# Kernel tuning notes

Hardware: AMD Instinct MI355X
Metric: run time of the kernel (lower is better)

Reference implementation:

```python
import jax, jax.numpy as jnp
import numpy as np


def _dF(field, c):
    """Central differences of component c of field [B,X,Y,Z,C] -> [B,X-2,Y-2,Z-2,3]."""
    f = field[..., c]
    dx = (f[:, 2:, 1:-1, 1:-1] - f[:, :-2, 1:-1, 1:-1]) * 0.5
    dy = (f[:, 1:-1, 2:, 1:-1] - f[:, 1:-1, :-2, 1:-1]) * 0.5
    dz = (f[:, 1:-1, 1:-1, 2:] - f[:, 1:-1, 1:-1, :-2]) * 0.5
    return jnp.stack((dx, dy, dz), axis=4)


def setup_inputs() -> dict:
    key = jax.random.key(0)
    grid = jax.random.normal(key, (2, 160, 160, 160, 3), dtype=jnp.float32)
    return {"grid": grid}


def reference(grid):
    # First derivatives of each displacement component: [B,X-2,Y-2,Z-2,3]
    dx = _dF(grid, 0)
    dy = _dF(grid, 1)
    dz = _dF(grid, 2)
    # Second derivatives: [B,X-4,Y-4,Z-4,3]
    dxx = _dF(dx, 0)
    dyy = _dF(dy, 1)
    dzz = _dF(dz, 2)
    dxy = _dF(dx, 1)
    dyz = _dF(dy, 2)
    dxz = _dF(dx, 2)
    penalty = jnp.sum(dxx ** 2 + dyy ** 2 + dzz ** 2
                      + 2.0 * (dxy ** 2 + dyz ** 2 + dxz ** 2))
    return penalty / dxx.size
```

## Files before the change

### kernel.cpp

```cpp
#include <hip/hip_runtime.h>

#define OY 480
#define OX 76800
#define SB 12288000
#define JT 12
#define KT 39
#define IT 39
#define NBLK 416
#define ROWF 129
#define RW 132
#define NROW 16
#define SLICE (NROW*RW)
#define NBUF 6
#define SLICE_FLOATS (NROW*ROWF)
#define PTS (JT*KT)
#define INV_SIZE (1.0f/22778496.0f)

__global__ __launch_bounds__(512)
void be_partials(const float* __restrict__ g, float* __restrict__ partial) {
    __shared__ float lds[NBUF * SLICE];
    __shared__ float wsum[8];

    const int tid = threadIdx.x;
    const int bid = blockIdx.x;
    const int kt  = bid & 3;
    const int is  = (bid >> 2) & 3;
    const int r   = bid >> 4;
    const int jt  = r % 13;
    const int bb  = r / 13;

    const int j0  = jt * JT;
    const int k0z = kt * KT;
    const int ib  = is * IT;

    const float* __restrict__ G = g + (size_t)bb * SB;

    int gd0, gd1, gd2, gd3, gd4 = 0, ld0, ld1, ld2, ld3, ld4 = 0;
    {
        int f, row, pos;
        f = tid;        row = f / ROWF; pos = f - row * ROWF;
        gd0 = (j0 + row) * OY + k0z * 3 + pos;  ld0 = row * RW + pos;
        f = tid + 512;  row = f / ROWF; pos = f - row * ROWF;
        gd1 = (j0 + row) * OY + k0z * 3 + pos;  ld1 = row * RW + pos;
        f = tid + 1024; row = f / ROWF; pos = f - row * ROWF;
        gd2 = (j0 + row) * OY + k0z * 3 + pos;  ld2 = row * RW + pos;
        f = tid + 1536; row = f / ROWF; pos = f - row * ROWF;
        gd3 = (j0 + row) * OY + k0z * 3 + pos;  ld3 = row * RW + pos;
    }
    const bool tail = (tid < SLICE_FLOATS - 2048);
    if (tail) {
        int f = tid + 2048; int row = f / ROWF; int pos = f - row * ROWF;
        gd4 = (j0 + row) * OY + k0z * 3 + pos;  ld4 = row * RW + pos;
    }

    const bool act = tid < PTS;
    int jj = tid / KT;
    int kk = tid - jj * KT;
    if (!act) { jj = 0; kk = 0; }
    const int cbase = (jj + 2) * RW + (kk + 2) * 3;

    #pragma unroll
    for (int w = 0; w < 5; ++w) {
        const int x = ib + w;
        const float* base = G + (size_t)x * OX;
        float a0 = base[gd0], a1 = base[gd1], a2 = base[gd2], a3 = base[gd3];
        float a4 = tail ? base[gd4] : 0.0f;
        float* L = lds + (x % NBUF) * SLICE;
        L[ld0] = a0; L[ld1] = a1; L[ld2] = a2; L[ld3] = a3;
        if (tail) L[ld4] = a4;
    }
    __syncthreads();

    float s = 0.0f;
    for (int i0 = ib; i0 < ib + IT; ++i0) {
        const int xn = i0 + 5;
        const bool doLoad = (xn <= ib + 42);
        float a0 = 0.f, a1 = 0.f, a2 = 0.f, a3 = 0.f, a4 = 0.f;
        if (doLoad) {
            const float* base = G + (size_t)xn * OX;
            a0 = base[gd0]; a1 = base[gd1]; a2 = base[gd2]; a3 = base[gd3];
            if (tail) a4 = base[gd4];
        }

        if (act) {
            int s0 = i0 % NBUF;
            int s1 = s0 + 1; if (s1 >= NBUF) s1 -= NBUF;
            int s2 = s1 + 1; if (s2 >= NBUF) s2 -= NBUF;
            int s3 = s2 + 1; if (s3 >= NBUF) s3 -= NBUF;
            int s4 = s3 + 1; if (s4 >= NBUF) s4 -= NBUF;
            const float* Sm2 = lds + s0 * SLICE + cbase;
            const float* Sm1 = lds + s1 * SLICE + cbase;
            const float* Sc  = lds + s2 * SLICE + cbase;
            const float* Sp1 = lds + s3 * SLICE + cbase;
            const float* Sp2 = lds + s4 * SLICE + cbase;

            const float c0 = Sc[0], c1 = Sc[1], c2 = Sc[2];
            float hzz0 = Sc[6] - 2.0f*c0 + Sc[-6];
            float hzz1 = Sc[7] - 2.0f*c1 + Sc[-5];
            float hzz2 = Sc[8] - 2.0f*c2 + Sc[-4];
            float hyy0 = Sc[ 2*RW]     - 2.0f*c0 + Sc[-2*RW];
            float hyy1 = Sc[ 2*RW + 1] - 2.0f*c1 + Sc[-2*RW + 1];
            float hxx0 = Sp2[0] - 2.0f*c0 + Sm2[0];
            float hyz0 = (Sc[RW+3] - Sc[RW-3]) - (Sc[-RW+3] - Sc[-RW-3]);
            float hyz1 = (Sc[RW+4] - Sc[RW-2]) - (Sc[-RW+4] - Sc[-RW-2]);
            float hyz2 = (Sc[RW+5] - Sc[RW-1]) - (Sc[-RW+5] - Sc[-RW-1]);
            float hxy0 = (Sp1[ RW]   - Sp1[-RW])   - (Sm1[ RW]   - Sm1[-RW]);
            float hxy1 = (Sp1[ RW+1] - Sp1[-RW+1]) - (Sm1[ RW+1] - Sm1[-RW+1]);
            float hxz0 = (Sp1[3] - Sp1[-3]) - (Sm1[3] - Sm1[-3]);
            float hxz1 = (Sp1[4] - Sp1[-2]) - (Sm1[4] - Sm1[-2]);
            float hxz2 = (Sp1[5] - Sp1[-1]) - (Sm1[5] - Sm1[-1]);

            float w1 = hxx0*hxx0;
            w1 = fmaf(hyy1, hyy1, w1); w1 = fmaf(hzz2, hzz2, w1);
            w1 = fmaf(hxy1, hxy1, w1); w1 = fmaf(hxz2, hxz2, w1);
            w1 = fmaf(hyz2, hyz2, w1);
            float w2 = hyy0*hyy0;
            w2 = fmaf(hzz0, hzz0, w2); w2 = fmaf(hzz1, hzz1, w2);
            w2 = fmaf(hxz1, hxz1, w2);
            float w3 = hxy0*hxy0;
            w3 = fmaf(hxz0, hxz0, w3); w3 = fmaf(hyz1, hyz1, w3);
            float w4 = hyz0*hyz0;

            float t = fmaf(2.0f, w2, w1);
            t = fmaf(3.0f, w3, t);
            t = fmaf(4.0f, w4, t);
            s = fmaf(0.0625f, t, s);
        }

        if (doLoad) {
            float* L = lds + (xn % NBUF) * SLICE;
            L[ld0] = a0; L[ld1] = a1; L[ld2] = a2; L[ld3] = a3;
            if (tail) L[ld4] = a4;
        }
        __syncthreads();
    }

    #pragma unroll
    for (int off = 32; off > 0; off >>= 1) s += __shfl_down(s, off, 64);
    if ((tid & 63) == 0) wsum[tid >> 6] = s;
    __syncthreads();
    if (tid == 0) {
        float tot = 0.0f;
        #pragma unroll
        for (int w = 0; w < 8; ++w) tot += wsum[w];
        partial[bid] = tot;
    }
}

__global__ __launch_bounds__(256)
void be_final(const float* __restrict__ partial, float* __restrict__ out) {
    float s = 0.0f;
    for (int i = threadIdx.x; i < NBLK; i += 256) s += partial[i];
    #pragma unroll
    for (int off = 32; off > 0; off >>= 1) s += __shfl_down(s, off, 64);
    __shared__ float ws[4];
    if ((threadIdx.x & 63) == 0) ws[threadIdx.x >> 6] = s;
    __syncthreads();
    if (threadIdx.x == 0)
        out[0] = ((ws[0] + ws[1]) + (ws[2] + ws[3])) * INV_SIZE;
}

extern "C" void kernel_launch(void* const* d_in, const int* in_sizes, int n_in,
                              void* d_out, int out_size, void* d_ws, size_t ws_size,
                              hipStream_t stream) {
    const float* grid = (const float*)d_in[0];
    float* out = (float*)d_out;
    float* partials = (float*)d_ws;

    be_partials<<<dim3(NBLK), dim3(512), 0, stream>>>(grid, partials);
    be_final<<<1, 256, 0, stream>>>(partials, out);
}
```

Measured before the change: 171.3 us.

## Restructure stencil with SoA LDS layout, double buffering, and x-derivative register reuse

Rewrites the partial kernel so global rows are loaded as float4 and transposed into a component-major (SoA) shared layout. The kernel now keeps only two slices in LDS and carries x-direction first differences and previous centre values in registers across steps instead of reading five slices. Each thread handles four z points with vectorised LDS reads, and the grid changes to 1014 blocks of 256 threads with shorter x-slabs. This is meant to cut LDS traffic and footprint and raise occupancy, at the cost of more halo reloading from shorter x-tiles and heavier register use.

```diff
diff --git a/kernel.cpp b/kernel.cpp
--- a/kernel.cpp
+++ b/kernel.cpp
@@ -4,147 +4,179 @@
 #define OX 76800
 #define SB 12288000
 #define JT 12
-#define KT 39
-#define IT 39
-#define NBLK 416
-#define ROWF 129
-#define RW 132
+#define KQ 13
+#define IT 12
 #define NROW 16
-#define SLICE (NROW*RW)
-#define NBUF 6
-#define SLICE_FLOATS (NROW*ROWF)
-#define PTS (JT*KT)
+#define ZST 60
+#define RST 180
+#define SLICE (NROW*RST)
+#define CTHR (JT*KQ)
+#define NGRP (NROW*14)
+#define NBLK 1014
 #define INV_SIZE (1.0f/22778496.0f)
 
-__global__ __launch_bounds__(512)
+__device__ __forceinline__ float4 ld4p(const float* p){ return *reinterpret_cast<const float4*>(p); }
+__device__ __forceinline__ float2 ld2p(const float* p){ return *reinterpret_cast<const float2*>(p); }
+__device__ __forceinline__ void st4p(float* p, float4 v){ *reinterpret_cast<float4*>(p) = v; }
+
+#define STEP(P, V0a, V0b, DP) { \
+    const int s = 2*d + (P); \
+    const bool doLoad = stg && (s <= 14); \
+    float4 A4, B4, C4; \
+    if (doLoad) { \
+        const float* gp = G + (size_t)(i0 - 1 + s)*OX + gbase; \
+        A4 = ld4p(gp); B4 = ld4p(gp+4); C4 = ld4p(gp+8); \
+    } \
+    if (act) { \
+        const bool doWS = (s >= 2) && (s <= 13); \
+        const bool doXY = (s >= 3) && (s <= 14); \
+        const bool doXX = (s >= 4); \
+        const float* L = lds + (P)*SLICE; \
+        float v0c[4], dz0[4], dz1[4], dz2[4], dyc0[4], dyc1[4]; \
+        {  \
+          float4 lo = ld4p(L+oj), hi = ld4p(L+oj+4); \
+          float f[8] = {lo.x,lo.y,lo.z,lo.w,hi.x,hi.y,hi.z,hi.w}; \
+          _Pragma("unroll") for (int v=0;v<4;++v){ v0c[v]=f[v+2]; dz0[v]=f[v+3]-f[v+1]; } \
+          if (doWS) { \
+            _Pragma("unroll") for (int v=0;v<4;++v){ float h=f[v+4]-2.f*f[v+2]+f[v]; cls2=fmaf(h,h,cls2); } \
+            float2 pa=ld2p(L+oj+2*RST+2), pb=ld2p(L+oj+2*RST+4); \
+            float2 ma=ld2p(L+oj-2*RST+2), mb=ld2p(L+oj-2*RST+4); \
+            float hp[4]={pa.x,pa.y,pb.x,pb.y}, hm[4]={ma.x,ma.y,mb.x,mb.y}; \
+            _Pragma("unroll") for (int v=0;v<4;++v){ float h=hp[v]-2.f*f[v+2]+hm[v]; cls2=fmaf(h,h,cls2); } \
+          } \
+        } \
+        {  \
+          float4 lo = ld4p(L+oj+ZST), hi = ld4p(L+oj+ZST+4); \
+          float f[8] = {lo.x,lo.y,lo.z,lo.w,hi.x,hi.y,hi.z,hi.w}; \
+          _Pragma("unroll") for (int v=0;v<4;++v){ dz1[v]=f[v+3]-f[v+1]; } \
+          if (doWS) { \
+            _Pragma("unroll") for (int v=0;v<4;++v){ float h=f[v+4]-2.f*f[v+2]+f[v]; cls2=fmaf(h,h,cls2); } \
+            float2 pa=ld2p(L+oj+2*RST+ZST+2), pb=ld2p(L+oj+2*RST+ZST+4); \
+            float2 ma=ld2p(L+oj-2*RST+ZST+2), mb=ld2p(L+oj-2*RST+ZST+4); \
+            float hp[4]={pa.x,pa.y,pb.x,pb.y}, hm[4]={ma.x,ma.y,mb.x,mb.y}; \
+            _Pragma("unroll") for (int v=0;v<4;++v){ float h=hp[v]-2.f*f[v+2]+hm[v]; cls1=fmaf(h,h,cls1); } \
+          } \
+        } \
+        {  \
+          float4 lo = ld4p(L+oj+2*ZST), hi = ld4p(L+oj+2*ZST+4); \
+          float f[8] = {lo.x,lo.y,lo.z,lo.w,hi.x,hi.y,hi.z,hi.w}; \
+          _Pragma("unroll") for (int v=0;v<4;++v){ dz2[v]=f[v+3]-f[v+1]; } \
+          if (doWS) { \
+            _Pragma("unroll") for (int v=0;v<4;++v){ float h=f[v+4]-2.f*f[v+2]+f[v]; cls1=fmaf(h,h,cls1); } \
+          } \
+        } \
+        {  \
+          float4 plo=ld4p(L+oj+RST), phi=ld4p(L+oj+RST+4); \
+          float4 mlo=ld4p(L+oj-RST), mhi=ld4p(L+oj-RST+4); \
+          float dyw[6]={plo.y-mlo.y, plo.z-mlo.z, plo.w-mlo.w, phi.x-mhi.x, phi.y-mhi.y, phi.z-mhi.z}; \
+          _Pragma("unroll") for (int v=0;v<4;++v) dyc0[v]=dyw[v+1]; \
+          if (doWS) { _Pragma("unroll") for (int v=0;v<4;++v){ float h=dyw[v+2]-dyw[v]; cls4=fmaf(h,h,cls4); } } \
+        } \
+        {  \
+          float4 plo=ld4p(L+oj+RST+ZST), phi=ld4p(L+oj+RST+ZST+4); \
+          float4 mlo=ld4p(L+oj-RST+ZST), mhi=ld4p(L+oj-RST+ZST+4); \
+          float dyw[6]={plo.y-mlo.y, plo.z-mlo.z, plo.w-mlo.w, phi.x-mhi.x, phi.y-mhi.y, phi.z-mhi.z}; \
+          _Pragma("unroll") for (int v=0;v<4;++v) dyc1[v]=dyw[v+1]; \
+          if (doWS) { _Pragma("unroll") for (int v=0;v<4;++v){ float h=dyw[v+2]-dyw[v]; cls3=fmaf(h,h,cls3); } } \
+        } \
+        if (doWS) {  \
+          float4 plo=ld4p(L+oj+RST+2*ZST), phi=ld4p(L+oj+RST+2*ZST+4); \
+          float4 mlo=ld4p(L+oj-RST+2*ZST), mhi=ld4p(L+oj-RST+2*ZST+4); \
+          float dyw[6]={plo.y-mlo.y, plo.z-mlo.z, plo.w-mlo.w, phi.x-mhi.x, phi.y-mhi.y, phi.z-mhi.z}; \
+          _Pragma("unroll") for (int v=0;v<4;++v){ float h=dyw[v+2]-dyw[v]; cls1=fmaf(h,h,cls1); } \
+        } \
+        _Pragma("unroll") for (int v=0;v<4;++v) { \
+          float o0=DP[0][v], o1=DP[1][v], o2=DP[2][v], o3=DP[3][v], o4=DP[4][v]; \
+          if (doXY) { float h; \
+            h=dyc0[v]-o0; cls3=fmaf(h,h,cls3); \
+            h=dyc1[v]-o1; cls1=fmaf(h,h,cls1); \
+            h=dz0[v]-o2;  cls3=fmaf(h,h,cls3); \
+            h=dz1[v]-o3;  cls2=fmaf(h,h,cls2); \
+            h=dz2[v]-o4;  cls1=fmaf(h,h,cls1); \
+          } \
+          DP[0][v]=dyc0[v]; DP[1][v]=dyc1[v]; DP[2][v]=dz0[v]; DP[3][v]=dz1[v]; DP[4][v]=dz2[v]; \
+          float w2v=V0a[v], w4v=V0b[v]; \
+          if (doXX) { float h=v0c[v]-2.f*w2v+w4v; cls1=fmaf(h,h,cls1); } \
+          V0b[v]=w2v; V0a[v]=v0c[v]; \
+        } \
+    } \
+    if (doLoad) { \
+        float* Lw = lds + ((P)^1)*SLICE + lbase; \
+        st4p(Lw,       make_float4(A4.x,A4.w,B4.z,C4.y)); \
+        st4p(Lw+ZST,   make_float4(A4.y,B4.x,B4.w,C4.z)); \
+        st4p(Lw+2*ZST, make_float4(A4.z,B4.y,C4.x,C4.w)); \
+    } \
+    __syncthreads(); \
+}
+
+__global__ __launch_bounds__(256)
 void be_partials(const float* __restrict__ g, float* __restrict__ partial) {
-    __shared__ float lds[NBUF * SLICE];
-    __shared__ float wsum[8];
+    __shared__ float lds[2*SLICE];
+    __shared__ float wsum[4];
 
     const int tid = threadIdx.x;
     const int bid = blockIdx.x;
-    const int kt  = bid & 3;
-    const int is  = (bid >> 2) & 3;
-    const int r   = bid >> 4;
-    const int jt  = r % 13;
-    const int bb  = r / 13;
-
-    const int j0  = jt * JT;
-    const int k0z = kt * KT;
-    const int ib  = is * IT;
-
-    const float* __restrict__ G = g + (size_t)bb * SB;
-
-    int gd0, gd1, gd2, gd3, gd4 = 0, ld0, ld1, ld2, ld3, ld4 = 0;
-    {
-        int f, row, pos;
-        f = tid;        row = f / ROWF; pos = f - row * ROWF;
-        gd0 = (j0 + row) * OY + k0z * 3 + pos;  ld0 = row * RW + pos;
-        f = tid + 512;  row = f / ROWF; pos = f - row * ROWF;
-        gd1 = (j0 + row) * OY + k0z * 3 + pos;  ld1 = row * RW + pos;
-        f = tid + 1024; row = f / ROWF; pos = f - row * ROWF;
-        gd2 = (j0 + row) * OY + k0z * 3 + pos;  ld2 = row * RW + pos;
-        f = tid + 1536; row = f / ROWF; pos = f - row * ROWF;
-        gd3 = (j0 + row) * OY + k0z * 3 + pos;  ld3 = row * RW + pos;
-    }
-    const bool tail = (tid < SLICE_FLOATS - 2048);
-    if (tail) {
-        int f = tid + 2048; int row = f / ROWF; int pos = f - row * ROWF;
-        gd4 = (j0 + row) * OY + k0z * 3 + pos;  ld4 = row * RW + pos;
-    }
-
-    const bool act = tid < PTS;
-    int jj = tid / KT;
-    int kk = tid - jj * KT;
-    if (!act) { jj = 0; kk = 0; }
-    const int cbase = (jj + 2) * RW + (kk + 2) * 3;
-
+    const int is = bid % 13;
+    int r1 = bid / 13;
+    const int kt = r1 % 3; r1 /= 3;
+    const int jt = r1 % 13;
+    const int bb = r1 / 13;
+
+    const int j0  = 2 + jt*JT;
+    const int zlo = 52*kt;
+    const int i0  = 2 + is*IT;
+    const float* __restrict__ G = g + (size_t)bb*SB;
+
+    const bool stg = tid < NGRP;
+    int gbase = 0, lbase = 0;
+    if (stg) {
+        int rr = tid/14, zq = tid - (tid/14)*14;
+        gbase = (j0-2+rr)*OY + (zlo+4*zq)*3;
+        lbase = rr*RST + 4*zq;
+    }
+
+    const bool act = tid < CTHR;
+    int cj = tid/KQ, cq = tid - (tid/KQ)*KQ;
+    if (!act) { cj = 0; cq = 0; }
+    const int oj = (cj+2)*RST + 4*cq;
+
+    float v0A0[4], v0A1[4], v0B0[4], v0B1[4];
+    float dpA[5][4], dpB[5][4];
     #pragma unroll
-    for (int w = 0; w < 5; ++w) {
-        const int x = ib + w;
-        const float* base = G + (size_t)x * OX;
-        float a0 = base[gd0], a1 = base[gd1], a2 = base[gd2], a3 = base[gd3];
-        float a4 = tail ? base[gd4] : 0.0f;
-        float* L = lds + (x % NBUF) * SLICE;
-        L[ld0] = a0; L[ld1] = a1; L[ld2] = a2; L[ld3] = a3;
-        if (tail) L[ld4] = a4;
+    for (int v=0;v<4;++v){
+        v0A0[v]=v0A1[v]=v0B0[v]=v0B1[v]=0.f;
+        #pragma unroll
+        for (int q=0;q<5;++q){ dpA[q][v]=0.f; dpB[q][v]=0.f; }
+    }
+    float cls1=0.f, cls2=0.f, cls3=0.f, cls4=0.f;
+
+    if (stg) {
+        const float* gp = G + (size_t)(i0-2)*OX + gbase;
+        float4 A4 = ld4p(gp), B4 = ld4p(gp+4), C4 = ld4p(gp+8);
+        float* Lw = lds + lbase;
+        st4p(Lw,       make_float4(A4.x,A4.w,B4.z,C4.y));
+        st4p(Lw+ZST,   make_float4(A4.y,B4.x,B4.w,C4.z));
+        st4p(Lw+2*ZST, make_float4(A4.z,B4.y,C4.x,C4.w));
     }
     __syncthreads();
 
-    float s = 0.0f;
-    for (int i0 = ib; i0 < ib + IT; ++i0) {
-        const int xn = i0 + 5;
-        const bool doLoad = (xn <= ib + 42);
-        float a0 = 0.f, a1 = 0.f, a2 = 0.f, a3 = 0.f, a4 = 0.f;
-        if (doLoad) {
-            const float* base = G + (size_t)xn * OX;
-            a0 = base[gd0]; a1 = base[gd1]; a2 = base[gd2]; a3 = base[gd3];
-            if (tail) a4 = base[gd4];
-        }
-
-        if (act) {
-            int s0 = i0 % NBUF;
-            int s1 = s0 + 1; if (s1 >= NBUF) s1 -= NBUF;
-            int s2 = s1 + 1; if (s2 >= NBUF) s2 -= NBUF;
-            int s3 = s2 + 1; if (s3 >= NBUF) s3 -= NBUF;
-            int s4 = s3 + 1; if (s4 >= NBUF) s4 -= NBUF;
-            const float* Sm2 = lds + s0 * SLICE + cbase;
-            const float* Sm1 = lds + s1 * SLICE + cbase;
-            const float* Sc  = lds + s2 * SLICE + cbase;
-            const float* Sp1 = lds + s3 * SLICE + cbase;
-            const float* Sp2 = lds + s4 * SLICE + cbase;
-
-            const float c0 = Sc[0], c1 = Sc[1], c2 = Sc[2];
-            float hzz0 = Sc[6] - 2.0f*c0 + Sc[-6];
-            float hzz1 = Sc[7] - 2.0f*c1 + Sc[-5];
-            float hzz2 = Sc[8] - 2.0f*c2 + Sc[-4];
-            float hyy0 = Sc[ 2*RW]     - 2.0f*c0 + Sc[-2*RW];
-            float hyy1 = Sc[ 2*RW + 1] - 2.0f*c1 + Sc[-2*RW + 1];
-            float hxx0 = Sp2[0] - 2.0f*c0 + Sm2[0];
-            float hyz0 = (Sc[RW+3] - Sc[RW-3]) - (Sc[-RW+3] - Sc[-RW-3]);
-            float hyz1 = (Sc[RW+4] - Sc[RW-2]) - (Sc[-RW+4] - Sc[-RW-2]);
-            float hyz2 = (Sc[RW+5] - Sc[RW-1]) - (Sc[-RW+5] - Sc[-RW-1]);
-            float hxy0 = (Sp1[ RW]   - Sp1[-RW])   - (Sm1[ RW]   - Sm1[-RW]);
-            float hxy1 = (Sp1[ RW+1] - Sp1[-RW+1]) - (Sm1[ RW+1] - Sm1[-RW+1]);
-            float hxz0 = (Sp1[3] - Sp1[-3]) - (Sm1[3] - Sm1[-3]);
-            float hxz1 = (Sp1[4] - Sp1[-2]) - (Sm1[4] - Sm1[-2]);
-            float hxz2 = (Sp1[5] - Sp1[-1]) - (Sm1[5] - Sm1[-1]);
-
-            float w1 = hxx0*hxx0;
-            w1 = fmaf(hyy1, hyy1, w1); w1 = fmaf(hzz2, hzz2, w1);
-            w1 = fmaf(hxy1, hxy1, w1); w1 = fmaf(hxz2, hxz2, w1);
-            w1 = fmaf(hyz2, hyz2, w1);
-            float w2 = hyy0*hyy0;
-            w2 = fmaf(hzz0, hzz0, w2); w2 = fmaf(hzz1, hzz1, w2);
-            w2 = fmaf(hxz1, hxz1, w2);
-            float w3 = hxy0*hxy0;
-            w3 = fmaf(hxz0, hxz0, w3); w3 = fmaf(hyz1, hyz1, w3);
-            float w4 = hyz0*hyz0;
-
-            float t = fmaf(2.0f, w2, w1);
-            t = fmaf(3.0f, w3, t);
-            t = fmaf(4.0f, w4, t);
-            s = fmaf(0.0625f, t, s);
-        }
-
-        if (doLoad) {
-            float* L = lds + (xn % NBUF) * SLICE;
-            L[ld0] = a0; L[ld1] = a1; L[ld2] = a2; L[ld3] = a3;
-            if (tail) L[ld4] = a4;
-        }
-        __syncthreads();
-    }
+    #pragma unroll 1
+    for (int d = 0; d < 8; ++d) {
+        STEP(0, v0A0, v0A1, dpA)
+        STEP(1, v0B0, v0B1, dpB)
+    }
+
+    float sv = fmaf(2.f, cls2, cls1);
+    sv = fmaf(3.f, cls3, sv);
+    sv = fmaf(4.f, cls4, sv);
+    sv *= 0.0625f;
 
     #pragma unroll
-    for (int off = 32; off > 0; off >>= 1) s += __shfl_down(s, off, 64);
-    if ((tid & 63) == 0) wsum[tid >> 6] = s;
+    for (int off = 32; off > 0; off >>= 1) sv += __shfl_down(sv, off, 64);
+    if ((tid & 63) == 0) wsum[tid >> 6] = sv;
     __syncthreads();
-    if (tid == 0) {
-        float tot = 0.0f;
-        #pragma unroll
-        for (int w = 0; w < 8; ++w) tot += wsum[w];
-        partial[bid] = tot;
-    }
+    if (tid == 0)
+        partial[bid] = (wsum[0] + wsum[1]) + (wsum[2] + wsum[3]);
 }
 
 __global__ __launch_bounds__(256)
@@ -167,6 +199,6 @@
     float* out = (float*)d_out;
     float* partials = (float*)d_ws;
 
-    be_partials<<<dim3(NBLK), dim3(512), 0, stream>>>(grid, partials);
+    be_partials<<<dim3(NBLK), dim3(256), 0, stream>>>(grid, partials);
     be_final<<<1, 256, 0, stream>>>(partials, out);
 }
```

Result: slower. 177.7 us (+3.8%).
